# Kernel tuning notes

Measured on AMD Instinct MI355X. Metric: run time of the kernel, lower is better.

The kernel has to match this reference:

```python
import jax, jax.numpy as jnp
from jax import lax
import numpy as np

EPS = 1e-5
# layer dims: (input_size, hidden_size) per bidirectional LSTM layer
LAYERS = [(7, 16), (32, 32), (64, 64), (128, 128)]
B, S = 64, 2048


def _run_lstm(x, Wih, Whh, bih, bhh):
    # x: [S, B, I]; Wih: [4H, I]; Whh: [4H, H]; gate order i, f, g, o (PyTorch)
    Bn = x.shape[1]
    H = Whh.shape[1]
    xW = jnp.einsum('sbi,gi->sbg', x, Wih) + bih + bhh  # [S, B, 4H]

    def step(carry, xw):
        h, c = carry
        g = xw + h @ Whh.T
        i, f, gg, o = jnp.split(g, 4, axis=-1)
        i = jax.nn.sigmoid(i)
        f = jax.nn.sigmoid(f)
        gg = jnp.tanh(gg)
        o = jax.nn.sigmoid(o)
        c = f * c + i * gg
        h = o * jnp.tanh(c)
        return (h, c), h

    h0 = jnp.zeros((Bn, H), x.dtype)
    _, hs = lax.scan(step, (h0, h0), xW)
    return hs  # [S, B, H]


def _bidir(x, Wih, Whh, bih, bhh):
    # weights stacked as [2, ...]: dir 0 = forward, dir 1 = backward
    hf = _run_lstm(x, Wih[0], Whh[0], bih[0], bhh[0])
    hb = _run_lstm(x[::-1], Wih[1], Whh[1], bih[1], bhh[1])[::-1]
    return jnp.concatenate([hf, hb], axis=-1)


def _bn(x, gamma, beta):
    # x: [S, B, C]; BatchNorm1d (training-mode batch stats) over (batch, time)
    mean = x.mean(axis=(0, 1))
    var = ((x - mean) ** 2).mean(axis=(0, 1))
    return gamma * (x - mean) * lax.rsqrt(var + EPS) + beta


def _forward(x, wih0, whh0, bih0, bhh0, wih1, whh1, bih1, bhh1,
             wih2, whh2, bih2, bhh2, wih3, whh3, bih3, bhh3,
             gamma0, beta0, gamma1, beta1, gamma2, beta2, gamma3, beta3,
             fc_w, fc_b):
    h = jnp.transpose(x, (1, 0, 2))  # [S, B, 7]
    lstm = [(wih0, whh0, bih0, bhh0), (wih1, whh1, bih1, bhh1),
            (wih2, whh2, bih2, bhh2), (wih3, whh3, bih3, bhh3)]
    bn = [(gamma0, beta0), (gamma1, beta1), (gamma2, beta2), (gamma3, beta3)]
    for (Wih, Whh, bih, bhh), (g, b) in zip(lstm, bn):
        h = _bidir(h, Wih, Whh, bih, bhh)
        h = _bn(h, g, b)
    h = jnp.transpose(h, (1, 0, 2))  # [B, S, 256]
    return h @ fc_w.T + fc_b  # [B, S, 11]


def setup_inputs() -> dict:
    key = jax.random.key(0)
    ks = iter(jax.random.split(key, 64))
    inp = {'x': jax.random.normal(next(ks), (B, S, 7), jnp.float32)}
    for li, (I, H) in enumerate(LAYERS):
        sc = 1.0 / np.sqrt(H)
        inp[f'wih{li}'] = jax.random.uniform(next(ks), (2, 4 * H, I), jnp.float32, -sc, sc)
        inp[f'whh{li}'] = jax.random.uniform(next(ks), (2, 4 * H, H), jnp.float32, -sc, sc)
        inp[f'bih{li}'] = jax.random.uniform(next(ks), (2, 4 * H), jnp.float32, -sc, sc)
        inp[f'bhh{li}'] = jax.random.uniform(next(ks), (2, 4 * H), jnp.float32, -sc, sc)
        inp[f'gamma{li}'] = jnp.ones((2 * H,), jnp.float32)
        inp[f'beta{li}'] = jnp.zeros((2 * H,), jnp.float32)
    sc = 1.0 / np.sqrt(256)
    inp['fc_w'] = jax.random.uniform(next(ks), (11, 256), jnp.float32, -sc, sc)
    inp['fc_b'] = jax.random.uniform(next(ks), (11,), jnp.float32, -sc, sc)
    return inp


def reference(x, wih0, whh0, bih0, bhh0, wih1, whh1, bih1, bhh1,
              wih2, whh2, bih2, bhh2, wih3, whh3, bih3, bhh3,
              gamma0, beta0, gamma1, beta1, gamma2, beta2, gamma3, beta3,
              fc_w, fc_b):
    return _forward(x, wih0, whh0, bih0, bhh0, wih1, whh1, bih1, bhh1,
                    wih2, whh2, bih2, bhh2, wih3, whh3, bih3, bhh3,
                    gamma0, beta0, gamma1, beta1, gamma2, beta2, gamma3, beta3,
                    fc_w, fc_b)
```

## Files before the change

### kernel.cpp

```cpp
#include <hip/hip_runtime.h>
#include <hip/hip_bf16.h>

#define DEVI __device__ __forceinline__

static constexpr int S = 2048;
static constexpr int B = 64;
static constexpr int M = S * B;

typedef __attribute__((ext_vector_type(8))) short bf16x8;
typedef __attribute__((ext_vector_type(4))) float f32x4;

DEVI float sigm(float x)   { return 1.0f / (1.0f + __expf(-x)); }
DEVI float tanh_f(float x) { return 1.0f - 2.0f / (1.0f + __expf(2.0f * x)); }

DEVI float ld1(const float* p) { return *p; }
DEVI float ld1(const __hip_bfloat16* p) { return __bfloat162float(*p); }
DEVI void  st1(float* p, float v) { *p = v; }
DEVI void  st1(__hip_bfloat16* p, float v) { *p = __float2bfloat16(v); }

DEVI float4 ld4(const float* p) { return *(const float4*)p; }
DEVI float4 ld4(const __hip_bfloat16* p) {
    const ushort4 u = *(const ushort4*)p;
    union { unsigned int i; float f; } a, b, c, d;
    a.i = (unsigned)u.x << 16; b.i = (unsigned)u.y << 16;
    c.i = (unsigned)u.z << 16; d.i = (unsigned)u.w << 16;
    return make_float4(a.f, b.f, c.f, d.f);
}

DEVI unsigned short f2bf(float v) { __hip_bfloat16 h = __float2bfloat16(v); return *(unsigned short*)&h; }

DEVI float shflf(float v, int lane) { return __shfl(v, lane, 64); }
DEVI float shflxf(float v, int mask) { return __shfl_xor(v, mask, 64); }

__global__ void zero_stats(float* stats) {
    stats[blockIdx.x * 256 + threadIdx.x] = 0.f;
}

template<typename XT, typename AT>
__global__ __launch_bounds__(256) void gemm_mfma(
    const AT* __restrict__ A, const float* __restrict__ W,
    const float* __restrict__ bih, const float* __restrict__ bhh,
    const float* __restrict__ scg_sb, XT* __restrict__ Xo,
    int K, int N, int mode, int t0f, int t0b, size_t halfElems)
{
    __shared__ __align__(16) unsigned short As[128][40];
    __shared__ __align__(16) unsigned short Bs[128][40];
    const int tid = threadIdx.x;
    const int m0 = blockIdx.x * 128;
    const int n0 = blockIdx.y * 128;
    const int dz = blockIdx.z;
    const int t0 = dz ? t0b : t0f;
    const float* Wd   = W   + (size_t)dz * N * K;
    const float* bihd = bih + (size_t)dz * N;
    const float* bhhd = bhh + (size_t)dz * N;
    XT* Xod = Xo + (size_t)dz * halfElems;
    const int l  = tid & 63, wid = tid >> 6;
    const int wm = wid >> 1, wn = wid & 1;

    f32x4 acc[4][4];
#pragma unroll
    for (int fm = 0; fm < 4; ++fm)
#pragma unroll
        for (int fn = 0; fn < 4; ++fn) acc[fm][fn] = (f32x4){0.f, 0.f, 0.f, 0.f};

    const int nks = (K + 31) / 32;
    for (int ks = 0; ks < nks; ++ks) {
        const int kc = ks * 32;
        if (mode == 1) {
#pragma unroll
            for (int it = 0; it < 4; ++it) {
                const int idx = it * 256 + tid;
                const int row = idx >> 3, k4 = (idx & 7) * 4;
                const int m = m0 + row;
                const size_t ma = (size_t)(t0 + (m >> 6)) * 64 + (m & 63);
                const float4 a4 = ld4(A + ma * K + kc + k4);
                const float4 g4 = *(const float4*)(scg_sb + kc + k4);
                const float4 b4 = *(const float4*)(scg_sb + K + kc + k4);
                ushort4 u;
                u.x = f2bf(a4.x * g4.x + b4.x); u.y = f2bf(a4.y * g4.y + b4.y);
                u.z = f2bf(a4.z * g4.z + b4.z); u.w = f2bf(a4.w * g4.w + b4.w);
                *(ushort4*)&As[row][k4] = u;
            }
        } else {
#pragma unroll
            for (int it = 0; it < 16; ++it) {
                const int idx = it * 256 + tid;
                const int row = idx >> 5, kk = idx & 31;
                const int m = m0 + row;
                float v = 0.f;
                if (kk < K)
                    v = ld1(A + ((size_t)(m & 63) * S + (t0 + (m >> 6))) * K + kk);
                As[row][kk] = f2bf(v);
            }
        }
        if (!(K & 3)) {
#pragma unroll
            for (int it = 0; it < 4; ++it) {
                const int idx = it * 256 + tid;
                const int row = idx >> 3, k4 = (idx & 7) * 4;
                const int n = n0 + row;
                float4 w4 = make_float4(0.f, 0.f, 0.f, 0.f);
                if (n < N) w4 = *(const float4*)(Wd + (size_t)n * K + kc + k4);
                ushort4 u;
                u.x = f2bf(w4.x); u.y = f2bf(w4.y); u.z = f2bf(w4.z); u.w = f2bf(w4.w);
                *(ushort4*)&Bs[row][k4] = u;
            }
        } else {
#pragma unroll
            for (int it = 0; it < 16; ++it) {
                const int idx = it * 256 + tid;
                const int row = idx >> 5, kk = idx & 31;
                const int n = n0 + row;
                float v = 0.f;
                if (n < N && kk < K) v = Wd[(size_t)n * K + kk];
                Bs[row][kk] = f2bf(v);
            }
        }
        __syncthreads();
        bf16x8 af[4], bw[4];
#pragma unroll
        for (int f = 0; f < 4; ++f) {
            af[f] = *(const bf16x8*)&As[wm * 64 + f * 16 + (l & 15)][(l >> 4) * 8];
            bw[f] = *(const bf16x8*)&Bs[wn * 64 + f * 16 + (l & 15)][(l >> 4) * 8];
        }
#pragma unroll
        for (int fm = 0; fm < 4; ++fm)
#pragma unroll
            for (int fn = 0; fn < 4; ++fn)
                acc[fm][fn] = __builtin_amdgcn_mfma_f32_16x16x32_bf16(af[fm], bw[fn], acc[fm][fn], 0, 0, 0);
        __syncthreads();
    }
#pragma unroll
    for (int fn = 0; fn < 4; ++fn) {
        const int n = n0 + wn * 64 + fn * 16 + (l & 15);
        if (n < N) {
            const float bias = bihd[n] + bhhd[n];
#pragma unroll
            for (int fm = 0; fm < 4; ++fm) {
                const int mr = m0 + wm * 64 + fm * 16 + (l >> 4) * 4;
#pragma unroll
                for (int r = 0; r < 4; ++r)
                    st1(Xod + (size_t)(mr + r) * N + n, acc[fm][fn][r] + bias);
            }
        }
    }
}

template<int PF, typename XT, typename AT>
__global__ __launch_bounds__(64, 1) void lstm_scan16(
    const XT* __restrict__ Xf, const XT* __restrict__ Xb_,
    AT* __restrict__ act, const float* __restrict__ whh,
    float* __restrict__ stats, float* __restrict__ state,
    int t0f, int tb_out, int CS, int first)
{
    const int l = threadIdx.x;
    const int dir = (blockIdx.x >= 64) ? 1 : 0;
    const int b = blockIdx.x & 63;
    const int u = l & 15;
    const int g4 = (l >> 4) * 4;

    float wi[4], wf_[4], wg[4], wo[4];
#pragma unroll
    for (int i = 0; i < 4; ++i) {
        wi[i]  = whh[(size_t)(dir * 64 +      u) * 16 + g4 + i];
        wf_[i] = whh[(size_t)(dir * 64 + 16 + u) * 16 + g4 + i];
        wg[i]  = whh[(size_t)(dir * 64 + 32 + u) * 16 + g4 + i];
        wo[i]  = whh[(size_t)(dir * 64 + 48 + u) * 16 + g4 + i];
    }

    const int sbase = (dir * 64 + b) * 32;
    float hv = 0.f, cc = 0.f, s1 = 0.f, s2 = 0.f;
    if (!first) { hv = state[sbase + u]; cc = state[sbase + 16 + u]; }

    const XT* Xd = (dir ? Xb_ : Xf) + (size_t)b * 64 + u;
    const size_t rstride = (size_t)64 * 64;
    float xw[PF][4];
#pragma unroll
    for (int p = 0; p < PF; ++p) {
        const size_t ro = (size_t)(dir ? (CS - 1 - p) : p) * rstride;
        xw[p][0] = ld1(Xd + ro);      xw[p][1] = ld1(Xd + ro + 16);
        xw[p][2] = ld1(Xd + ro + 32); xw[p][3] = ld1(Xd + ro + 48);
    }

    for (int tb = 0; tb < CS; tb += PF) {
#pragma unroll
        for (int p = 0; p < PF; ++p) {
            const int pstep = tb + p;
            const float h0 = shflf(hv, g4 + 0);
            const float h1 = shflf(hv, g4 + 1);
            const float h2 = shflf(hv, g4 + 2);
            const float h3 = shflf(hv, g4 + 3);
            float gi = h0 * wi[0]  + h1 * wi[1]  + h2 * wi[2]  + h3 * wi[3];
            float gf = h0 * wf_[0] + h1 * wf_[1] + h2 * wf_[2] + h3 * wf_[3];
            float gg = h0 * wg[0]  + h1 * wg[1]  + h2 * wg[2]  + h3 * wg[3];
            float go = h0 * wo[0]  + h1 * wo[1]  + h2 * wo[2]  + h3 * wo[3];
            gi += shflxf(gi, 16); gi += shflxf(gi, 32);
            gf += shflxf(gf, 16); gf += shflxf(gf, 32);
            gg += shflxf(gg, 16); gg += shflxf(gg, 32);
            go += shflxf(go, 16); go += shflxf(go, 32);
            gi += xw[p][0]; gf += xw[p][1]; gg += xw[p][2]; go += xw[p][3];
            if (pstep + PF < CS) {
                const size_t ro = (size_t)(dir ? (CS - 1 - (pstep + PF)) : (pstep + PF)) * rstride;
                xw[p][0] = ld1(Xd + ro);      xw[p][1] = ld1(Xd + ro + 16);
                xw[p][2] = ld1(Xd + ro + 32); xw[p][3] = ld1(Xd + ro + 48);
            }
            cc = sigm(gf) * cc + sigm(gi) * tanh_f(gg);
            hv = sigm(go) * tanh_f(cc);
            if (l < 16) {
                AT hq; st1(&hq, hv);
                const float hs = ld1(&hq);
                const int tt = dir ? (tb_out - pstep) : (t0f + pstep);
                act[((size_t)tt * B + b) * 32 + dir * 16 + l] = hq;
                s1 += hs; s2 += hs * hs;
            }
        }
    }
    if (l < 16) {
        state[sbase + l] = hv;
        state[sbase + 16 + l] = cc;
        atomicAdd(stats + dir * 16 + l, s1);
        atomicAdd(stats + 32 + dir * 16 + l, s2);
    }
}

template<int PF, typename XT, typename AT>
__global__ __launch_bounds__(64, 1) void lstm_scan32(
    const XT* __restrict__ Xf, const XT* __restrict__ Xb_,
    AT* __restrict__ act, const float* __restrict__ whh,
    float* __restrict__ stats, float* __restrict__ state,
    int t0f, int tb_out, int CS, int first)
{
    const int j = threadIdx.x;
    const int dir = (blockIdx.x >= 64) ? 1 : 0;
    const int b = blockIdx.x & 63;
    const int u = j & 31;

    float w0[32], w1[32];
#pragma unroll
    for (int k = 0; k < 32; ++k) {
        w0[k] = whh[(size_t)(dir * 128 + j) * 32 + k];
        w1[k] = whh[(size_t)(dir * 128 + 64 + j) * 32 + k];
    }

    const int sbase = (dir * 64 + b) * 64;
    float hv = 0.f, cc = 0.f, s1 = 0.f, s2 = 0.f;
    if (!first) { hv = state[sbase + u]; cc = state[sbase + 32 + u]; }

    const XT* Xd = (dir ? Xb_ : Xf) + (size_t)b * 128 + j;
    const size_t rstride = (size_t)64 * 128;
    float xwA[PF], xwB[PF];
#pragma unroll
    for (int p = 0; p < PF; ++p) {
        const size_t ro = (size_t)(dir ? (CS - 1 - p) : p) * rstride;
        xwA[p] = ld1(Xd + ro); xwB[p] = ld1(Xd + ro + 64);
    }

    for (int tb = 0; tb < CS; tb += PF) {
#pragma unroll
        for (int p = 0; p < PF; ++p) {
            const int pstep = tb + p;
            float gA = xwA[p], gB = xwB[p];
#pragma unroll
            for (int k = 0; k < 32; ++k) {
                const float s = shflf(hv, k);
                gA += s * w0[k]; gB += s * w1[k];
            }
            if (pstep + PF < CS) {
                const size_t ro = (size_t)(dir ? (CS - 1 - (pstep + PF)) : (pstep + PF)) * rstride;
                xwA[p] = ld1(Xd + ro); xwB[p] = ld1(Xd + ro + 64);
            }
            const float iv = shflf(gA, u);
            const float fv = shflf(gA, u + 32);
            const float gv = shflf(gB, u);
            const float ov = shflf(gB, u + 32);
            cc = sigm(fv) * cc + sigm(iv) * tanh_f(gv);
            hv = sigm(ov) * tanh_f(cc);
            if (j < 32) {
                AT hq; st1(&hq, hv);
                const float hs = ld1(&hq);
                const int tt = dir ? (tb_out - pstep) : (t0f + pstep);
                act[((size_t)tt * B + b) * 64 + dir * 32 + j] = hq;
                s1 += hs; s2 += hs * hs;
            }
        }
    }
    if (j < 32) {
        state[sbase + j] = hv;
        state[sbase + 32 + j] = cc;
        atomicAdd(stats + dir * 32 + j, s1);
        atomicAdd(stats + 64 + dir * 32 + j, s2);
    }
}

template<int H, int R, int PF, typename XT, typename AT>
__global__ __launch_bounds__(4 * H / R, 1) void lstm_scan(
    const XT* __restrict__ Xf, const XT* __restrict__ Xb_,
    AT* __restrict__ act, const float* __restrict__ whh,
    float* __restrict__ stats, float* __restrict__ state,
    int t0f, int tb_out, int CS, int first)
{
    constexpr int N4 = 4 * H;
    constexpr int T  = N4 / R;
    constexpr int CO = 2 * H;
    const int j   = threadIdx.x;
    const int dir = (blockIdx.x >= 64) ? 1 : 0;
    const int b   = blockIdx.x & 63;

    __shared__ __align__(16) float h_lds[H];
    __shared__ float g_lds[N4];

    float w[R][H];
#pragma unroll
    for (int r = 0; r < R; ++r)
#pragma unroll
        for (int k = 0; k < H; ++k)
            w[r][k] = whh[((size_t)dir * N4 + j + r * T) * H + k];

    const int sbase = (dir * 64 + b) * 2 * H;
    float cc = 0.f, s1 = 0.f, s2 = 0.f;
    if (j < H) {
        float h0 = 0.f;
        if (!first) { h0 = state[sbase + j]; cc = state[sbase + H + j]; }
        h_lds[j] = h0;
    }
    __syncthreads();

    const XT* Xd = (dir ? Xb_ : Xf) + (size_t)b * N4 + j;
    const size_t rstride = (size_t)64 * N4;

    float xw[PF][R];
#pragma unroll
    for (int p = 0; p < PF; ++p) {
        const int row = dir ? (CS - 1 - p) : p;
#pragma unroll
        for (int r = 0; r < R; ++r)
            xw[p][r] = ld1(Xd + (size_t)row * rstride + r * T);
    }

    for (int tb = 0; tb < CS; tb += PF) {
#pragma unroll
        for (int p = 0; p < PF; ++p) {
            const int pstep = tb + p;
            float acc0[R], acc1[R], acc2[R], acc3[R];
#pragma unroll
            for (int r = 0; r < R; ++r) { acc0[r] = 0.f; acc1[r] = 0.f; acc2[r] = 0.f; acc3[r] = 0.f; }
            const float4* h4 = (const float4*)h_lds;
#pragma unroll
            for (int k4 = 0; k4 < H / 4; ++k4) {
                const float4 hv = h4[k4];
#pragma unroll
                for (int r = 0; r < R; ++r) {
                    acc0[r] += w[r][4 * k4 + 0] * hv.x;
                    acc1[r] += w[r][4 * k4 + 1] * hv.y;
                    acc2[r] += w[r][4 * k4 + 2] * hv.z;
                    acc3[r] += w[r][4 * k4 + 3] * hv.w;
                }
            }
            float g[R];
#pragma unroll
            for (int r = 0; r < R; ++r)
                g[r] = (acc0[r] + acc1[r]) + (acc2[r] + acc3[r]) + xw[p][r];
            if (pstep + PF < CS) {
                const int row = dir ? (CS - 1 - (pstep + PF)) : (pstep + PF);
#pragma unroll
                for (int r = 0; r < R; ++r)
                    xw[p][r] = ld1(Xd + (size_t)row * rstride + r * T);
            }
#pragma unroll
            for (int r = 0; r < R; ++r) g_lds[j + r * T] = g[r];
            __syncthreads();
            if (j < H) {
                const float fi = sigm(g_lds[j]);
                const float ff = sigm(g_lds[H + j]);
                const float fg = tanh_f(g_lds[2 * H + j]);
                const float fo = sigm(g_lds[3 * H + j]);
                cc = ff * cc + fi * fg;
                const float hv = fo * tanh_f(cc);
                h_lds[j] = hv;
                AT hq; st1(&hq, hv);
                const float hs = ld1(&hq);
                const int tt = dir ? (tb_out - pstep) : (t0f + pstep);
                act[((size_t)tt * B + b) * CO + dir * H + j] = hq;
                s1 += hs; s2 += hs * hs;
            }
            __syncthreads();
        }
    }
    if (j < H) {
        state[sbase + j]     = h_lds[j];
        state[sbase + H + j] = cc;
        atomicAdd(stats + dir * H + j, s1);
        atomicAdd(stats + CO + dir * H + j, s2);
    }
}

template<int PF, typename XT, typename AT>
__global__ __launch_bounds__(1024, 1) void lstm_scan128(
    const XT* __restrict__ Xf, const XT* __restrict__ Xb_,
    AT* __restrict__ act, const float* __restrict__ whh,
    float* __restrict__ stats, float* __restrict__ state,
    int t0f, int tb_out, int CS, int first)
{
    const int tid = threadIdx.x;
    const int j   = tid & 511;
    const int kh  = tid >> 9;
    const int dir = (blockIdx.x >= 64) ? 1 : 0;
    const int b   = blockIdx.x & 63;

    __shared__ __align__(16) float h_lds[128];
    __shared__ __align__(16) float psum[2][512];

    float w[64];
#pragma unroll
    for (int k = 0; k < 64; ++k)
        w[k] = whh[((size_t)dir * 512 + j) * 128 + kh * 64 + k];

    const int sbase = (dir * 64 + b) * 256;
    float cc = 0.f, s1 = 0.f, s2 = 0.f;
    if (tid < 128) {
        float h0 = 0.f;
        if (!first) { h0 = state[sbase + tid]; cc = state[sbase + 128 + tid]; }
        h_lds[tid] = h0;
    }
    __syncthreads();

    const XT* Xd = (dir ? Xb_ : Xf) + (size_t)b * 512 + j;
    const size_t rstride = (size_t)64 * 512;

    float xw[PF];
    if (kh == 0) {
#pragma unroll
        for (int p = 0; p < PF; ++p) {
            const int row = dir ? (CS - 1 - p) : p;
            xw[p] = ld1(Xd + (size_t)row * rstride);
        }
    }

    for (int tb = 0; tb < CS; tb += PF) {
#pragma unroll
        for (int p = 0; p < PF; ++p) {
            const int pstep = tb + p;
            float a0 = 0.f, a1 = 0.f, a2 = 0.f, a3 = 0.f;
            const float4* h4 = (const float4*)&h_lds[kh * 64];
#pragma unroll
            for (int k4 = 0; k4 < 16; ++k4) {
                const float4 hv = h4[k4];
                a0 += w[4 * k4 + 0] * hv.x;
                a1 += w[4 * k4 + 1] * hv.y;
                a2 += w[4 * k4 + 2] * hv.z;
                a3 += w[4 * k4 + 3] * hv.w;
            }
            float partial = (a0 + a1) + (a2 + a3);
            if (kh == 0) {
                partial += xw[p];
                if (pstep + PF < CS) {
                    const int row = dir ? (CS - 1 - (pstep + PF)) : (pstep + PF);
                    xw[p] = ld1(Xd + (size_t)row * rstride);
                }
            }
            psum[kh][j] = partial;
            __syncthreads();
            if (tid < 128) {
                const int u = tid;
                const float gi = psum[0][u]       + psum[1][u];
                const float gf = psum[0][128 + u] + psum[1][128 + u];
                const float gg = psum[0][256 + u] + psum[1][256 + u];
                const float go = psum[0][384 + u] + psum[1][384 + u];
                cc = sigm(gf) * cc + sigm(gi) * tanh_f(gg);
                const float hvv = sigm(go) * tanh_f(cc);
                h_lds[u] = hvv;
                AT hq; st1(&hq, hvv);
                const float hs = ld1(&hq);
                const int tt = dir ? (tb_out - pstep) : (t0f + pstep);
                act[((size_t)tt * B + b) * 256 + dir * 128 + u] = hq;
                s1 += hs; s2 += hs * hs;
            }
            __syncthreads();
        }
    }
    if (tid < 128) {
        state[sbase + tid]       = h_lds[tid];
        state[sbase + 128 + tid] = cc;
        atomicAdd(stats + dir * 128 + tid, s1);
        atomicAdd(stats + 256 + dir * 128 + tid, s2);
    }
}

__global__ void bn_finalize(const float* __restrict__ sums, float* __restrict__ scg_sb,
                            const float* __restrict__ gamma, const float* __restrict__ beta,
                            int CO)
{
    const int c = threadIdx.x;
    if (c < CO) {
        const float inv  = 1.0f / (float)M;
        const float mean = sums[c] * inv;
        const float var  = fmaxf(sums[CO + c] * inv - mean * mean, 0.f);
        const float s    = gamma[c] * rsqrtf(var + 1e-5f);
        scg_sb[c]      = s;
        scg_sb[CO + c] = beta[c] - mean * s;
    }
}

template<typename AT>
__global__ __launch_bounds__(256) void fc_kernel(
    const AT* __restrict__ act, const float* __restrict__ scg_sb,
    const float* __restrict__ fc_w, const float* __restrict__ fc_b,
    float* __restrict__ out)
{
    __shared__ __align__(16) float a_s[32][264];
    __shared__ __align__(16) float w_s[11][264];
    const int tid = threadIdx.x;
    const int m0  = blockIdx.x * 32;
#pragma unroll
    for (int u = 0; u < 12; ++u) {
        int q = u * 256 + tid;
        int uu = q >> 8, c = q & 255;
        if (uu < 11) w_s[uu][c] = fc_w[uu * 256 + c];
    }
#pragma unroll
    for (int u = 0; u < 8; ++u) {
        int q = u * 256 + tid;
        int r = q >> 6, c4 = q & 63;
        const float4 a4 = ld4(act + (size_t)(m0 + r) * 256 + c4 * 4);
        const float4 g4 = *(const float4*)(scg_sb + c4 * 4);
        const float4 b4 = *(const float4*)(scg_sb + 256 + c4 * 4);
        float4 v;
        v.x = a4.x * g4.x + b4.x; v.y = a4.y * g4.y + b4.y;
        v.z = a4.z * g4.z + b4.z; v.w = a4.w * g4.w + b4.w;
        *(float4*)&a_s[r][c4 * 4] = v;
    }
    __syncthreads();
    const int r = tid >> 3, jj = tid & 7;
    const size_t m = (size_t)m0 + r;
    float* orow = out + ((m & 63) * S + (m >> 6)) * 11;
#pragma unroll
    for (int jv = 0; jv < 2; ++jv) {
        const int j = jj + jv * 8;
        if (j < 11) {
            float a0 = 0, a1 = 0, a2 = 0, a3 = 0;
#pragma unroll
            for (int c4 = 0; c4 < 64; ++c4) {
                const float4 av = *(const float4*)&a_s[r][c4 * 4];
                const float4 wv = *(const float4*)&w_s[j][c4 * 4];
                a0 += av.x * wv.x; a1 += av.y * wv.y;
                a2 += av.z * wv.z; a3 += av.w * wv.w;
            }
            orow[j] = (a0 + a1) + (a2 + a3) + fc_b[j];
        }
    }
}

template<int H, typename XT, typename AT, typename AIN>
static void run_layer(const AIN* A, const float* wih, const float* whh,
                      const float* bih, const float* bhh,
                      const float* scg_prev, AT* act_out,
                      float* stats_l, float* state, XT* Xbuf,
                      int K, int mode, int CS, hipStream_t stream)
{
    const int N4 = 4 * H, P = S / CS;
    const size_t half = (size_t)CS * 64 * N4;
    XT* Xf = Xbuf;
    XT* Xb = Xbuf + half;
    const dim3 gg(CS * 64 / 128, (N4 + 127) / 128, 2);
    for (int jc = 0; jc < P; ++jc) {
        gemm_mfma<XT, AIN><<<gg, 256, 0, stream>>>(
            A, wih, bih, bhh, scg_prev, Xf, K, N4, mode,
            jc * CS, S - (jc + 1) * CS, half);
        if constexpr (H == 16)
            lstm_scan16<4, XT, AT><<<128, 64, 0, stream>>>(
                Xf, Xb, act_out, whh, stats_l, state, jc * CS, S - 1 - jc * CS, CS, jc == 0);
        else if constexpr (H == 32)
            lstm_scan32<4, XT, AT><<<128, 64, 0, stream>>>(
                Xf, Xb, act_out, whh, stats_l, state, jc * CS, S - 1 - jc * CS, CS, jc == 0);
        else if constexpr (H == 128)
            lstm_scan128<4, XT, AT><<<128, 1024, 0, stream>>>(
                Xf, Xb, act_out, whh, stats_l, state, jc * CS, S - 1 - jc * CS, CS, jc == 0);
        else
            lstm_scan<H, 1, 4, XT, AT><<<128, 4 * H, 0, stream>>>(
                Xf, Xb, act_out, whh, stats_l, state, jc * CS, S - 1 - jc * CS, CS, jc == 0);
    }
}

template<typename XT, typename AT>
static void run_all(void* const* d_in, float* out, float* stats, float* state,
                    AT* actA, AT* actB, XT* Xbuf, const int* CS, hipStream_t stream)
{
    auto in = [&](int i) { return (const float*)d_in[i]; };
    zero_stats<<<16, 256, 0, stream>>>(stats);

    run_layer<16, XT, AT, float>((const float*)d_in[0], in(1), in(2), in(3), in(4),
                                 nullptr, actA, stats + 0, state, Xbuf, 7, 0, CS[0], stream);
    bn_finalize<<<1, 256, 0, stream>>>(stats + 0, stats + 512, in(5), in(6), 32);

    run_layer<32, XT, AT, AT>(actA, in(7), in(8), in(9), in(10),
                              stats + 512, actB, stats + 1024, state, Xbuf, 32, 1, CS[1], stream);
    bn_finalize<<<1, 256, 0, stream>>>(stats + 1024, stats + 1536, in(11), in(12), 64);

    run_layer<64, XT, AT, AT>(actB, in(13), in(14), in(15), in(16),
                              stats + 1536, actA, stats + 2048, state, Xbuf, 64, 1, CS[2], stream);
    bn_finalize<<<1, 256, 0, stream>>>(stats + 2048, stats + 2560, in(17), in(18), 128);

    run_layer<128, XT, AT, AT>(actA, in(19), in(20), in(21), in(22),
                               stats + 2560, actB, stats + 3072, state, Xbuf, 128, 1, CS[3], stream);
    bn_finalize<<<1, 256, 0, stream>>>(stats + 3072, stats + 3584, in(23), in(24), 256);

    fc_kernel<AT><<<M / 32, 256, 0, stream>>>(actB, stats + 3584, in(25), in(26), out);
}

static inline int fit_cs(size_t xavail, size_t bytes_per_step) {
    for (int cs = 2048; cs >= 64; cs >>= 1)
        if ((size_t)cs * bytes_per_step <= xavail) return cs;
    return 64;
}

extern "C" void kernel_launch(void* const* d_in, const int* in_sizes, int n_in,
                              void* d_out, int out_size, void* d_ws, size_t ws_size,
                              hipStream_t stream)
{
    (void)in_sizes; (void)n_in; (void)out_size;
    float* out = (float*)d_out;
    char* ws = (char*)d_ws;
    const size_t STB  = 16384;
    const size_t STT  = 131072;
    const size_t HEAD = STB + STT;
    const size_t AAf  = (size_t)M * 128 * 4;
    const size_t ABf  = (size_t)M * 256 * 4;
    const size_t XF3  = (size_t)M * 1024 * 4;
    const size_t XGOOD = (size_t)140 * 1024 * 1024;
    const int H8[4] = {128, 256, 512, 1024};

    float* stats = (float*)ws;
    float* state = (float*)(ws + STB);
    char*  bufs  = ws + HEAD;
    int CS[4];

    if (ws_size >= HEAD + AAf + ABf + XF3) {
        float* actA = (float*)bufs;
        float* actB = (float*)(bufs + AAf);
        float* X    = (float*)(bufs + AAf + ABf);
        const size_t xavail = ws_size - HEAD - AAf - ABf;
        for (int l = 0; l < 4; ++l) CS[l] = fit_cs(xavail, (size_t)64 * H8[l] * 4);
        run_all<float, float>(d_in, out, stats, state, actA, actB, X, CS, stream);
    } else if (ws_size >= HEAD + AAf + ABf + XGOOD) {
        float* actA = (float*)bufs;
        float* actB = (float*)(bufs + AAf);
        __hip_bfloat16* X = (__hip_bfloat16*)(bufs + AAf + ABf);
        const size_t xavail = ws_size - HEAD - AAf - ABf;
        for (int l = 0; l < 4; ++l) CS[l] = fit_cs(xavail, (size_t)64 * H8[l] * 2);
        run_all<__hip_bfloat16, float>(d_in, out, stats, state, actA, actB, X, CS, stream);
    } else {
        __hip_bfloat16* actA = (__hip_bfloat16*)bufs;
        __hip_bfloat16* actB = (__hip_bfloat16*)(bufs + AAf / 2);
        __hip_bfloat16* X    = (__hip_bfloat16*)(bufs + AAf / 2 + ABf / 2);
        const size_t used = HEAD + AAf / 2 + ABf / 2;
        const size_t xavail = (ws_size > used) ? (ws_size - used) : 0;
        for (int l = 0; l < 4; ++l) CS[l] = fit_cs(xavail, (size_t)64 * H8[l] * 2);
        run_all<__hip_bfloat16, __hip_bfloat16>(d_in, out, stats, state, actA, actB, X, CS, stream);
    }
}
```

Baseline: 7.231 ms.

## Add split-K H=64 LSTM scan and broadcast hidden state via readlane

Replaces the generic H=64 scan (256 threads, each holding a full 64-wide weight row) with a dedicated 512-thread kernel that splits the K dimension in two halves and combines the partial sums through shared memory. In both the H=64 and H=128 scans, each lane now holds one hidden-state element in a register, and the matvec broadcasts it with readlane instead of reading float4 vectors from LDS. The aim is shorter per-step dependency chains and fewer LDS reads on the serial recurrence path. The cost is more threads per block plus an extra partial-sum reduction, and readlane emits scalar-lane instructions whose throughput may not beat LDS broadcast reads.

```diff
diff --git a/kernel.cpp b/kernel.cpp
--- a/kernel.cpp
+++ b/kernel.cpp
@@ -29,6 +29,9 @@
 
 DEVI unsigned short f2bf(float v) { __hip_bfloat16 h = __float2bfloat16(v); return *(unsigned short*)&h; }
 
+DEVI float bcastf(float v, int lane) {
+    return __int_as_float(__builtin_amdgcn_readlane(__float_as_int(v), lane));
+}
 DEVI float shflf(float v, int lane) { return __shfl(v, lane, 64); }
 DEVI float shflxf(float v, int mask) { return __shfl_xor(v, mask, 64); }
 
@@ -292,105 +295,96 @@
     }
 }
 
-template<int H, int R, int PF, typename XT, typename AT>
-__global__ __launch_bounds__(4 * H / R, 1) void lstm_scan(
+template<int PF, typename XT, typename AT>
+__global__ __launch_bounds__(512, 1) void lstm_scan64(
     const XT* __restrict__ Xf, const XT* __restrict__ Xb_,
     AT* __restrict__ act, const float* __restrict__ whh,
     float* __restrict__ stats, float* __restrict__ state,
     int t0f, int tb_out, int CS, int first)
 {
-    constexpr int N4 = 4 * H;
-    constexpr int T  = N4 / R;
-    constexpr int CO = 2 * H;
-    const int j   = threadIdx.x;
+    const int tid = threadIdx.x;
+    const int j   = tid & 255;
+    const int kh  = tid >> 8;
+    const int l   = tid & 63;
     const int dir = (blockIdx.x >= 64) ? 1 : 0;
     const int b   = blockIdx.x & 63;
 
-    __shared__ __align__(16) float h_lds[H];
-    __shared__ float g_lds[N4];
-
-    float w[R][H];
-#pragma unroll
-    for (int r = 0; r < R; ++r)
-#pragma unroll
-        for (int k = 0; k < H; ++k)
-            w[r][k] = whh[((size_t)dir * N4 + j + r * T) * H + k];
-
-    const int sbase = (dir * 64 + b) * 2 * H;
+    __shared__ __align__(16) float h_lds[64];
+    __shared__ __align__(16) float psum[2][256];
+
+    float w[32];
+#pragma unroll
+    for (int k = 0; k < 32; ++k)
+        w[k] = whh[((size_t)dir * 256 + j) * 64 + kh * 32 + k];
+
+    const int sbase = (dir * 64 + b) * 128;
     float cc = 0.f, s1 = 0.f, s2 = 0.f;
-    if (j < H) {
+    if (tid < 64) {
         float h0 = 0.f;
-        if (!first) { h0 = state[sbase + j]; cc = state[sbase + H + j]; }
-        h_lds[j] = h0;
+        if (!first) { h0 = state[sbase + tid]; cc = state[sbase + 64 + tid]; }
+        h_lds[tid] = h0;
     }
     __syncthreads();
-
-    const XT* Xd = (dir ? Xb_ : Xf) + (size_t)b * N4 + j;
-    const size_t rstride = (size_t)64 * N4;
-
-    float xw[PF][R];
-#pragma unroll
-    for (int p = 0; p < PF; ++p) {
-        const int row = dir ? (CS - 1 - p) : p;
-#pragma unroll
-        for (int r = 0; r < R; ++r)
-            xw[p][r] = ld1(Xd + (size_t)row * rstride + r * T);
+    float hreg = h_lds[kh * 32 + (l & 31)];
+
+    const XT* Xd = (dir ? Xb_ : Xf) + (size_t)b * 256 + j;
+    const size_t rstride = (size_t)64 * 256;
+
+    float xw[PF];
+    if (kh == 0) {
+#pragma unroll
+        for (int p = 0; p < PF; ++p) {
+            const int row = dir ? (CS - 1 - p) : p;
+            xw[p] = ld1(Xd + (size_t)row * rstride);
+        }
     }
 
     for (int tb = 0; tb < CS; tb += PF) {
 #pragma unroll
         for (int p = 0; p < PF; ++p) {
             const int pstep = tb + p;
-            float acc0[R], acc1[R], acc2[R], acc3[R];
-#pragma unroll
-            for (int r = 0; r < R; ++r) { acc0[r] = 0.f; acc1[r] = 0.f; acc2[r] = 0.f; acc3[r] = 0.f; }
-            const float4* h4 = (const float4*)h_lds;
-#pragma unroll
-            for (int k4 = 0; k4 < H / 4; ++k4) {
-                const float4 hv = h4[k4];
-#pragma unroll
-                for (int r = 0; r < R; ++r) {
-                    acc0[r] += w[r][4 * k4 + 0] * hv.x;
-                    acc1[r] += w[r][4 * k4 + 1] * hv.y;
-                    acc2[r] += w[r][4 * k4 + 2] * hv.z;
-                    acc3[r] += w[r][4 * k4 + 3] * hv.w;
+            float a0 = 0.f, a1 = 0.f, a2 = 0.f, a3 = 0.f;
+#pragma unroll
+            for (int k4 = 0; k4 < 8; ++k4) {
+                a0 += bcastf(hreg, 4 * k4 + 0) * w[4 * k4 + 0];
+                a1 += bcastf(hreg, 4 * k4 + 1) * w[4 * k4 + 1];
+                a2 += bcastf(hreg, 4 * k4 + 2) * w[4 * k4 + 2];
+                a3 += bcastf(hreg, 4 * k4 + 3) * w[4 * k4 + 3];
+            }
+            float partial = (a0 + a1) + (a2 + a3);
+            if (kh == 0) {
+                partial += xw[p];
+                if (pstep + PF < CS) {
+                    const int row = dir ? (CS - 1 - (pstep + PF)) : (pstep + PF);
+                    xw[p] = ld1(Xd + (size_t)row * rstride);
                 }
             }
-            float g[R];
-#pragma unroll
-            for (int r = 0; r < R; ++r)
-                g[r] = (acc0[r] + acc1[r]) + (acc2[r] + acc3[r]) + xw[p][r];
-            if (pstep + PF < CS) {
-                const int row = dir ? (CS - 1 - (pstep + PF)) : (pstep + PF);
-#pragma unroll
-                for (int r = 0; r < R; ++r)
-                    xw[p][r] = ld1(Xd + (size_t)row * rstride + r * T);
-            }
-#pragma unroll
-            for (int r = 0; r < R; ++r) g_lds[j + r * T] = g[r];
+            psum[kh][j] = partial;
             __syncthreads();
-            if (j < H) {
-                const float fi = sigm(g_lds[j]);
-                const float ff = sigm(g_lds[H + j]);
-                const float fg = tanh_f(g_lds[2 * H + j]);
-                const float fo = sigm(g_lds[3 * H + j]);
-                cc = ff * cc + fi * fg;
-                const float hv = fo * tanh_f(cc);
-                h_lds[j] = hv;
-                AT hq; st1(&hq, hv);
+            if (tid < 64) {
+                const int u = tid;
+                const float gi = psum[0][u]       + psum[1][u];
+                const float gf = psum[0][64 + u]  + psum[1][64 + u];
+                const float gg = psum[0][128 + u] + psum[1][128 + u];
+                const float go = psum[0][192 + u] + psum[1][192 + u];
+                cc = sigm(gf) * cc + sigm(gi) * tanh_f(gg);
+                const float hvv = sigm(go) * tanh_f(cc);
+                h_lds[u] = hvv;
+                AT hq; st1(&hq, hvv);
                 const float hs = ld1(&hq);
                 const int tt = dir ? (tb_out - pstep) : (t0f + pstep);
-                act[((size_t)tt * B + b) * CO + dir * H + j] = hq;
+                act[((size_t)tt * B + b) * 128 + dir * 64 + u] = hq;
                 s1 += hs; s2 += hs * hs;
             }
             __syncthreads();
-        }
-    }
-    if (j < H) {
-        state[sbase + j]     = h_lds[j];
-        state[sbase + H + j] = cc;
-        atomicAdd(stats + dir * H + j, s1);
-        atomicAdd(stats + CO + dir * H + j, s2);
+            hreg = h_lds[kh * 32 + (l & 31)];
+        }
+    }
+    if (tid < 64) {
+        state[sbase + tid]      = h_lds[tid];
+        state[sbase + 64 + tid] = cc;
+        atomicAdd(stats + dir * 64 + tid, s1);
+        atomicAdd(stats + 128 + dir * 64 + tid, s2);
     }
 }
 
@@ -404,6 +398,7 @@
     const int tid = threadIdx.x;
     const int j   = tid & 511;
     const int kh  = tid >> 9;
+    const int l   = tid & 63;
     const int dir = (blockIdx.x >= 64) ? 1 : 0;
     const int b   = blockIdx.x & 63;
 
@@ -423,6 +418,7 @@
         h_lds[tid] = h0;
     }
     __syncthreads();
+    float hreg = h_lds[kh * 64 + l];
 
     const XT* Xd = (dir ? Xb_ : Xf) + (size_t)b * 512 + j;
     const size_t rstride = (size_t)64 * 512;
@@ -441,14 +437,12 @@
         for (int p = 0; p < PF; ++p) {
             const int pstep = tb + p;
             float a0 = 0.f, a1 = 0.f, a2 = 0.f, a3 = 0.f;
-            const float4* h4 = (const float4*)&h_lds[kh * 64];
 #pragma unroll
             for (int k4 = 0; k4 < 16; ++k4) {
-                const float4 hv = h4[k4];
-                a0 += w[4 * k4 + 0] * hv.x;
-                a1 += w[4 * k4 + 1] * hv.y;
-                a2 += w[4 * k4 + 2] * hv.z;
-                a3 += w[4 * k4 + 3] * hv.w;
+                a0 += bcastf(hreg, 4 * k4 + 0) * w[4 * k4 + 0];
+                a1 += bcastf(hreg, 4 * k4 + 1) * w[4 * k4 + 1];
+                a2 += bcastf(hreg, 4 * k4 + 2) * w[4 * k4 + 2];
+                a3 += bcastf(hreg, 4 * k4 + 3) * w[4 * k4 + 3];
             }
             float partial = (a0 + a1) + (a2 + a3);
             if (kh == 0) {
@@ -476,6 +470,7 @@
                 s1 += hs; s2 += hs * hs;
             }
             __syncthreads();
+            hreg = h_lds[kh * 64 + l];
         }
     }
     if (tid < 128) {
@@ -572,11 +567,11 @@
         else if constexpr (H == 32)
             lstm_scan32<4, XT, AT><<<128, 64, 0, stream>>>(
                 Xf, Xb, act_out, whh, stats_l, state, jc * CS, S - 1 - jc * CS, CS, jc == 0);
-        else if constexpr (H == 128)
-            lstm_scan128<4, XT, AT><<<128, 1024, 0, stream>>>(
+        else if constexpr (H == 64)
+            lstm_scan64<4, XT, AT><<<128, 512, 0, stream>>>(
                 Xf, Xb, act_out, whh, stats_l, state, jc * CS, S - 1 - jc * CS, CS, jc == 0);
         else
-            lstm_scan<H, 1, 4, XT, AT><<<128, 4 * H, 0, stream>>>(
+            lstm_scan128<4, XT, AT><<<128, 1024, 0, stream>>>(
                 Xf, Xb, act_out, whh, stats_l, state, jc * CS, S - 1 - jc * CS, CS, jc == 0);
     }
 }
```

Measured after the change: 6.938 ms. -4.0%, faster.
